# Kernel tuning notes

Measured on AMD Instinct MI355X. Metric: run time of the kernel, lower is better.

The kernel has to match this reference:

```python
import jax, jax.numpy as jnp
import numpy as np
import math

DIM = 512
HEADS = 8          # dim // num_head_channels = 512 // 64
HEAD_CH = 64
GROUPS = 32        # guided-diffusion normalization() = GroupNorm(32, dim)
EPS = 1e-5
CROSS_DIM = 768


def setup_inputs() -> dict:
    key = jax.random.key(0)
    ks = jax.random.split(key, 8)
    B, C, Hs, Ws, L = 16, DIM, 32, 32, 77
    x = jax.random.normal(ks[0], (B, C, Hs, Ws), dtype=jnp.float32)
    c = jax.random.normal(ks[1], (B, CROSS_DIM, L), dtype=jnp.float32)
    # GroupNorm affine params
    gamma = jnp.ones((C,), jnp.float32)
    beta = jnp.zeros((C,), jnp.float32)
    # 1x1 conv weights stored as [out, in]
    w_qkv = jax.random.normal(ks[2], (3 * C, C), jnp.float32) / math.sqrt(C)
    b_qkv = jnp.zeros((3 * C,), jnp.float32)
    w_c = jax.random.normal(ks[3], (2 * C, CROSS_DIM), jnp.float32) / math.sqrt(CROSS_DIM)
    b_c = jnp.zeros((2 * C,), jnp.float32)
    # NOTE: original proj_out is zero-initialized (zero_module); we use small
    # random weights so the reference exercises non-trivial math end-to-end.
    w_p = jax.random.normal(ks[4], (C, C), jnp.float32) / math.sqrt(C)
    b_p = jnp.zeros((C,), jnp.float32)
    return {"x": x, "c": c, "gamma": gamma, "beta": beta,
            "w_qkv": w_qkv, "b_qkv": b_qkv, "w_c": w_c, "b_c": b_c,
            "w_p": w_p, "b_p": b_p}


def reference(x, c, gamma, beta, w_qkv, b_qkv, w_c, b_c, w_p, b_p):
    B, C, Hs, Ws = x.shape
    T = Hs * Ws
    xf = x.reshape(B, C, T)

    # GroupNorm(32) over (channels_per_group, spatial)
    xg = xf.reshape(B, GROUPS, C // GROUPS, T)
    mean = xg.mean(axis=(2, 3), keepdims=True)
    var = xg.var(axis=(2, 3), keepdims=True)
    xn = ((xg - mean) * jax.lax.rsqrt(var + EPS)).reshape(B, C, T)
    xn = xn * gamma[None, :, None] + beta[None, :, None]

    # qkv 1x1 conv: [B, 3C, T]
    qkv = jnp.einsum('oc,bct->bot', w_qkv, xn) + b_qkv[None, :, None]
    q, k, v = jnp.split(qkv, 3, axis=1)
    q = q.reshape(B, HEADS, HEAD_CH, T)
    k = k.reshape(B, HEADS, HEAD_CH, T)
    v = v.reshape(B, HEADS, HEAD_CH, T)

    # cross-attn cond kv: [B, 2C, L] -> concat on sequence axis
    ckv = jnp.einsum('oc,bcl->bol', w_c, c) + b_c[None, :, None]
    kc, vc = jnp.split(ckv, 2, axis=1)
    L = c.shape[-1]
    k = jnp.concatenate([k, kc.reshape(B, HEADS, HEAD_CH, L)], axis=-1)
    v = jnp.concatenate([v, vc.reshape(B, HEADS, HEAD_CH, L)], axis=-1)

    scale = 1.0 / math.sqrt(HEAD_CH)
    # scores [B, H, T, T+L]; scale applied inside softmax as in FusedSoftmaxMaybeApex
    logits = jnp.einsum('bhct,bhcs->bhts', q, k) * scale
    w = jax.nn.softmax(logits, axis=-1)
    a = jnp.einsum('bhts,bhcs->bhct', w, v).reshape(B, C, T)

    h = jnp.einsum('oc,bct->bot', w_p, a) + b_p[None, :, None]
    return (xf + h).reshape(B, C, Hs, Ws)
```

## Files before the change

kernel.cpp:

```cpp
#include <hip/hip_runtime.h>

#define B_   16
#define C_   512
#define T_   1024
#define H_   8
#define D_   64
#define G_   32
#define L_   77
#define S_   1101
#define SPAD 1152
#define NPAD 51
#define CD_  768
#define BT_  (B_*T_)
#define BL_  (B_*L_)
#define KROW 72
#define QSC  0.18033688011112042f

typedef __bf16 bf16x8 __attribute__((ext_vector_type(8)));
typedef float  f32x4  __attribute__((ext_vector_type(4)));

static __device__ __forceinline__ unsigned short f2bf(float f) {
    unsigned int u = __float_as_uint(f);
    u = (u + 0x7fffu + ((u >> 16) & 1u)) >> 16;
    return (unsigned short)u;
}

static __device__ __forceinline__ void gload_lds16(const unsigned short* g,
                                                   unsigned short* l) {
    __builtin_amdgcn_global_load_lds(
        (const __attribute__((address_space(1))) unsigned int*)g,
        (__attribute__((address_space(3))) unsigned int*)l, 16, 0, 0);
}

__global__ __launch_bounds__(256) void prep_k(const float* __restrict__ x,
                                              float* __restrict__ stats,
                                              const float* __restrict__ w_qkv,
                                              const float* __restrict__ w_p,
                                              const float* __restrict__ w_c,
                                              unsigned short* __restrict__ wqkv_pk,
                                              unsigned short* __restrict__ wp_pk,
                                              unsigned short* __restrict__ wc_pk) {
    const int tid = threadIdx.x;
    if (blockIdx.x < 512) {
        const int bg = blockIdx.x;
        const float* p = x + (size_t)bg * 16384;
        float s = 0.f, s2 = 0.f;
        for (int i = tid; i < 16384; i += 256) {
            float v = p[i];
            s += v; s2 += v * v;
        }
        __shared__ float rs[256], rs2[256];
        rs[tid] = s; rs2[tid] = s2;
        __syncthreads();
        for (int off = 128; off > 0; off >>= 1) {
            if (tid < off) { rs[tid] += rs[tid + off]; rs2[tid] += rs2[tid + off]; }
            __syncthreads();
        }
        if (tid == 0) {
            float mean = rs[0] * (1.0f / 16384.0f);
            float var  = rs2[0] * (1.0f / 16384.0f) - mean * mean;
            stats[2 * bg]     = mean;
            stats[2 * bg + 1] = rsqrtf(var + 1e-5f);
        }
        return;
    }
    const int cid = (blockIdx.x - 512) * 256 + tid;
    const float* src;
    unsigned short* dst;
    if (cid < 98304) {
        const int ml = cid & 127, k8 = (cid >> 7) & 7, kt = (cid >> 10) & 7, mt = cid >> 13;
        src = w_qkv + (size_t)(mt * 128 + ml) * 512 + kt * 64 + k8 * 8;
        dst = wqkv_pk + (size_t)cid * 8;
    } else if (cid < 131072) {
        const int c2 = cid - 98304;
        const int ml = c2 & 127, k8 = (c2 >> 7) & 7, kt = (c2 >> 10) & 7, mt = c2 >> 13;
        src = w_p + (size_t)(mt * 128 + ml) * 512 + kt * 64 + k8 * 8;
        dst = wp_pk + (size_t)c2 * 8;
    } else {
        const int c3 = cid - 131072;
        const int ml = c3 & 127, k8 = (c3 >> 7) & 7;
        const int ktmt = c3 >> 10;
        const int kt = ktmt % 12, mt = ktmt / 12;
        src = w_c + (size_t)(mt * 128 + ml) * 768 + kt * 64 + k8 * 8;
        dst = wc_pk + (size_t)c3 * 8;
    }
    const float4 v0 = *(const float4*)src, v1 = *(const float4*)(src + 4);
    unsigned short tmp[8];
    tmp[0] = f2bf(v0.x); tmp[1] = f2bf(v0.y); tmp[2] = f2bf(v0.z); tmp[3] = f2bf(v0.w);
    tmp[4] = f2bf(v1.x); tmp[5] = f2bf(v1.y); tmp[6] = f2bf(v1.z); tmp[7] = f2bf(v1.w);
    *(uint4*)dst = *(uint4*)tmp;
}

__global__ __launch_bounds__(256) void gn_apply_t(const float* __restrict__ x,
                                                  const float* __restrict__ stats,
                                                  const float* __restrict__ gamma,
                                                  const float* __restrict__ beta,
                                                  unsigned short* __restrict__ xnT) {
    const int t0 = blockIdx.x * 64, kt = blockIdx.y, b = blockIdx.z;
    const int c0 = kt * 64;
    const int tid = threadIdx.x;
    __shared__ float st[64][66];
#pragma unroll
    for (int it = 0; it < 4; it++) {
        const int fid = it * 256 + tid;
        const int ci = fid >> 4, t4 = (fid & 15) * 4;
        const int c = c0 + ci;
        const float4 xv = *(const float4*)&x[((size_t)(b * C_ + c) << 10) + t0 + t4];
        const int bg = b * G_ + (c >> 4);
        const float mean = stats[2 * bg], istd = stats[2 * bg + 1];
        const float gs = gamma[c] * istd, gb = beta[c] - mean * gs;
        st[t4 + 0][ci] = xv.x * gs + gb;
        st[t4 + 1][ci] = xv.y * gs + gb;
        st[t4 + 2][ci] = xv.z * gs + gb;
        st[t4 + 3][ci] = xv.w * gs + gb;
    }
    __syncthreads();
#pragma unroll
    for (int it = 0; it < 2; it++) {
        const int cid = it * 256 + tid;
        const int k8 = cid >> 6, tl = cid & 63;
        const int n = (b << 10) + t0 + tl;
        const int nt = n >> 7, nm = n & 127;
        unsigned short tmp[8];
        const float* src = &st[tl][k8 * 8];
#pragma unroll
        for (int q = 0; q < 8; q++) tmp[q] = f2bf(src[q]);
        *(uint4*)&xnT[(((size_t)nt * 8 + kt) * 8 + k8) * 1024 + (size_t)nm * 8] = *(uint4*)tmp;
    }
}

__global__ __launch_bounds__(256) void pack_c_k(const float* __restrict__ c,
                                                unsigned short* __restrict__ cpk) {
    const int kt = blockIdx.x, b = blockIdx.y;
#pragma unroll
    for (int it = 0; it < 4; it++) {
        const int idx = it * 256 + threadIdx.x;
        const int k8 = idx >> 7, l = idx & 127;
        unsigned short tmp[8];
        const float* src = c + ((size_t)b * CD_ + kt * 64 + k8 * 8) * L_ + l;
#pragma unroll
        for (int q = 0; q < 8; q++)
            tmp[q] = (l < L_) ? f2bf(src[(size_t)q * L_]) : (unsigned short)0;
        *(uint4*)&cpk[(size_t)b * 98304 + ((size_t)(kt * 8 + k8)) * 1024 + (size_t)l * 8] =
            *(uint4*)tmp;
    }
}

template<int MODE, int KT>
__global__ __launch_bounds__(256) void mgemm_k(const unsigned short* __restrict__ Apk,
                                               const unsigned short* __restrict__ Bpk,
                                               const float* __restrict__ bias,
                                               const float* __restrict__ resid,
                                               unsigned short* __restrict__ qb,
                                               unsigned short* __restrict__ kb,
                                               unsigned short* __restrict__ vb,
                                               float* __restrict__ outp) {
    __shared__ unsigned short lds[16896];
    const int tid = threadIdx.x, wave = tid >> 6, lane = tid & 63;
    const int quad = lane >> 4, l16 = lane & 15;
    const int nt = blockIdx.x, mt = blockIdx.y;
    const int mw = (wave & 1) * 64, nw = (wave >> 1) * 64;

    f32x4 acc[4][4];
#pragma unroll
    for (int i = 0; i < 4; i++)
#pragma unroll
        for (int j = 0; j < 4; j++) acc[i][j] = (f32x4){0.f, 0.f, 0.f, 0.f};

    const unsigned short* Ab = Apk + (size_t)mt * KT * 8192;
    const unsigned short* Bb = Bpk + ((MODE == 2) ? (size_t)blockIdx.z * KT * 8192 : 0)
                                   + (size_t)nt * KT * 8192;

    for (int kt = 0; kt < KT; kt++) {
        const unsigned short* as = Ab + kt * 8192 + wave * 2048 + lane * 8;
        const unsigned short* bs = Bb + kt * 8192 + wave * 2048 + lane * 8;
        unsigned short* la = lds + wave * 2048;
        unsigned short* lb = lds + 8192 + wave * 2048;
#pragma unroll
        for (int j = 0; j < 4; j++) {
            gload_lds16(as + j * 512, la + j * 512);
            gload_lds16(bs + j * 512, lb + j * 512);
        }
        __syncthreads();
#pragma unroll
        for (int kh = 0; kh < 2; kh++) {
            const int k8 = kh * 4 + quad;
            bf16x8 af[4], bfr[4];
#pragma unroll
            for (int i = 0; i < 4; i++) {
                af[i]  = *(const bf16x8*)&lds[(size_t)(k8 * 128 + mw + i * 16 + l16) * 8];
                bfr[i] = *(const bf16x8*)&lds[8192 + (size_t)(k8 * 128 + nw + i * 16 + l16) * 8];
            }
#pragma unroll
            for (int mi = 0; mi < 4; mi++)
#pragma unroll
                for (int ni = 0; ni < 4; ni++)
                    acc[mi][ni] = __builtin_amdgcn_mfma_f32_16x16x32_bf16(
                        af[mi], bfr[ni], acc[mi][ni], 0, 0, 0);
        }
        __syncthreads();
    }

    const int gm0 = mt * 128 + mw;
    const int gn0 = nt * 128 + nw;

    if (MODE == 0) {
        const int region = gm0 >> 9;
        const int o0 = gm0 & 511;
        const int h = o0 >> 6;
        const int b = gn0 >> 10, t0 = gn0 & 1023;
        const int bh = b * 8 + h;
        unsigned short* wlds = lds + wave * 4224;
        if (region < 2) {
            const float sc = (region == 0) ? QSC : 1.0f;
#pragma unroll
            for (int mi = 0; mi < 4; mi++)
#pragma unroll
                for (int ni = 0; ni < 4; ni++)
#pragma unroll
                    for (int r = 0; r < 4; r++) {
                        const float v = (acc[mi][ni][r] + bias[gm0 + mi * 16 + quad * 4 + r]) * sc;
                        wlds[(ni * 16 + l16) * 66 + mi * 16 + quad * 4 + r] = f2bf(v);
                    }
            __syncthreads();
            unsigned short* dst = (region == 0)
                ? qb + ((size_t)bh * 1024 + t0) * 64
                : kb + ((size_t)bh * SPAD + t0) * 64;
            const int ch8 = lane & 7, tb = lane >> 3;
#pragma unroll
            for (int it = 0; it < 8; it++) {
                const int tl = it * 8 + tb;
                *(uint4*)&dst[(size_t)tl * 64 + ch8 * 8] = *(const uint4*)&wlds[tl * 66 + ch8 * 8];
            }
        } else {
#pragma unroll
            for (int mi = 0; mi < 4; mi++)
#pragma unroll
                for (int ni = 0; ni < 4; ni++)
#pragma unroll
                    for (int r = 0; r < 4; r++) {
                        const float v = acc[mi][ni][r] + bias[gm0 + mi * 16 + quad * 4 + r];
                        wlds[(mi * 16 + quad * 4 + r) * 66 + ni * 16 + l16] = f2bf(v);
                    }
            __syncthreads();
            const int s8 = lane & 7, cb = lane >> 3;
#pragma unroll
            for (int it = 0; it < 8; it++) {
                const int ch = it * 8 + cb;
                *(uint4*)&vb[((size_t)bh * 64 + ch) * SPAD + t0 + s8 * 8] =
                    *(const uint4*)&wlds[ch * 66 + s8 * 8];
            }
        }
    } else if (MODE == 1) {
        const int b = gn0 >> 10, t0 = gn0 & 1023;
#pragma unroll
        for (int mi = 0; mi < 4; mi++) {
#pragma unroll
            for (int r = 0; r < 4; r++) {
                const int m = gm0 + mi * 16 + quad * 4 + r;
                const float bv = bias[m];
                const size_t rowb = ((size_t)(b * C_ + m) << 10) + t0;
#pragma unroll
                for (int ni = 0; ni < 4; ni++) {
                    const size_t a = rowb + ni * 16 + l16;
                    outp[a] = acc[mi][ni][r] + bv + resid[a];
                }
            }
        }
    } else {
        const int region = gm0 >> 9;
        const int o0 = gm0 & 511;
        const int h = o0 >> 6;
        const int b = blockIdx.z;
        const int bh = b * 8 + h;
        unsigned short* wlds = lds + wave * 4224;
        if (region == 0) {
#pragma unroll
            for (int mi = 0; mi < 4; mi++)
#pragma unroll
                for (int ni = 0; ni < 4; ni++) {
                    const bool valid = (gn0 + ni * 16 + l16) < L_;
#pragma unroll
                    for (int r = 0; r < 4; r++) {
                        const float v = valid ? acc[mi][ni][r] + bias[gm0 + mi * 16 + quad * 4 + r] : 0.f;
                        wlds[(ni * 16 + l16) * 66 + mi * 16 + quad * 4 + r] = f2bf(v);
                    }
                }
            __syncthreads();
            unsigned short* dst = kb + ((size_t)bh * SPAD + 1024 + gn0) * 64;
            const int ch8 = lane & 7, tb = lane >> 3;
#pragma unroll
            for (int it = 0; it < 8; it++) {
                const int tl = it * 8 + tb;
                *(uint4*)&dst[(size_t)tl * 64 + ch8 * 8] = *(const uint4*)&wlds[tl * 66 + ch8 * 8];
            }
        } else {
#pragma unroll
            for (int mi = 0; mi < 4; mi++)
#pragma unroll
                for (int ni = 0; ni < 4; ni++) {
                    const bool valid = (gn0 + ni * 16 + l16) < L_;
#pragma unroll
                    for (int r = 0; r < 4; r++) {
                        const float v = valid ? acc[mi][ni][r] + bias[gm0 + mi * 16 + quad * 4 + r] : 0.f;
                        wlds[(mi * 16 + quad * 4 + r) * 66 + ni * 16 + l16] = f2bf(v);
                    }
                }
            __syncthreads();
            const int s8 = lane & 7, cb = lane >> 3;
#pragma unroll
            for (int it = 0; it < 8; it++) {
                const int ch = it * 8 + cb;
                *(uint4*)&vb[((size_t)bh * 64 + ch) * SPAD + 1024 + gn0 + s8 * 8] =
                    *(const uint4*)&wlds[ch * 66 + s8 * 8];
            }
        }
    }
}

__global__ __launch_bounds__(256) void flash_k(const unsigned short* __restrict__ qb,
                                               const unsigned short* __restrict__ kb,
                                               const unsigned short* __restrict__ vb,
                                               unsigned short* __restrict__ aT) {
    __shared__ __align__(16) unsigned short qs[64 * KROW];
    __shared__ __align__(16) unsigned short ks[64 * KROW];
    __shared__ __align__(16) unsigned short vs[64 * KROW];

    const int tid  = threadIdx.x;
    const int wave = tid >> 6, lane = tid & 63;
    const int quad = lane >> 4, l16 = lane & 15;
    const int bh  = blockIdx.x;
    const int b = bh >> 3, h = bh & 7;
    const int qt0 = blockIdx.y * 64;

    {
        const int row = tid >> 2, col = (tid & 3) * 16;
        const unsigned short* src = qb + ((size_t)bh * 1024 + qt0) * 64;
        *(uint4*)&qs[row * KROW + col]     = *(const uint4*)&src[row * 64 + col];
        *(uint4*)&qs[row * KROW + col + 8] = *(const uint4*)&src[row * 64 + col + 8];
    }
    const int qrow = wave * 16 + l16;
    const bf16x8 aq0 = *(const bf16x8*)&qs[qrow * KROW + quad * 8];
    const bf16x8 aq1 = *(const bf16x8*)&qs[qrow * KROW + 32 + quad * 8];

    unsigned short* ps = qs + wave * 16 * KROW;

    float rsum[4] = {0.f, 0.f, 0.f, 0.f};
    f32x4 o_acc[4];
#pragma unroll
    for (int nb = 0; nb < 4; nb++) o_acc[nb] = (f32x4){0.f, 0.f, 0.f, 0.f};

    for (int s0 = 0; s0 < SPAD; s0 += 64) {
        __syncthreads();
        {
            const int row = tid >> 2, col = (tid & 3) * 16;
            const unsigned short* ksrc = kb + ((size_t)bh * SPAD + s0 + row) * 64;
            *(uint4*)&ks[row * KROW + col]     = *(const uint4*)&ksrc[col];
            *(uint4*)&ks[row * KROW + col + 8] = *(const uint4*)&ksrc[col + 8];
            const unsigned short* vsrc = vb + ((size_t)bh * 64 + row) * SPAD + s0;
            *(uint4*)&vs[row * KROW + col]     = *(const uint4*)&vsrc[col];
            *(uint4*)&vs[row * KROW + col + 8] = *(const uint4*)&vsrc[col + 8];
        }
        __syncthreads();

        f32x4 sacc[4];
#pragma unroll
        for (int cb = 0; cb < 4; cb++) {
            const bf16x8 bk0 = *(const bf16x8*)&ks[(cb * 16 + l16) * KROW + quad * 8];
            const bf16x8 bk1 = *(const bf16x8*)&ks[(cb * 16 + l16) * KROW + 32 + quad * 8];
            f32x4 z = (f32x4){0.f, 0.f, 0.f, 0.f};
            z = __builtin_amdgcn_mfma_f32_16x16x32_bf16(aq0, bk0, z, 0, 0, 0);
            z = __builtin_amdgcn_mfma_f32_16x16x32_bf16(aq1, bk1, z, 0, 0, 0);
            sacc[cb] = z;
        }

#pragma unroll
        for (int cb = 0; cb < 4; cb++) {
#pragma unroll
            for (int r = 0; r < 4; r++) {
                const float e = __builtin_exp2f(sacc[cb][r]);
                rsum[r] += e;
                ps[(quad * 4 + r) * 64 + ((cb * 16 + l16 + 16 * quad) & 63)] = f2bf(e);
            }
        }
        asm volatile("s_waitcnt lgkmcnt(0)" ::: "memory");

        const int pc0 = (quad * 8 + 16 * (l16 >> 2)) & 63;
        const int pc1 = (32 + quad * 8 + 16 * (l16 >> 2)) & 63;
        const bf16x8 ap0 = *(const bf16x8*)&ps[l16 * 64 + pc0];
        const bf16x8 ap1 = *(const bf16x8*)&ps[l16 * 64 + pc1];
#pragma unroll
        for (int nb = 0; nb < 4; nb++) {
            const bf16x8 bv0 = *(const bf16x8*)&vs[(nb * 16 + l16) * KROW + quad * 8];
            const bf16x8 bv1 = *(const bf16x8*)&vs[(nb * 16 + l16) * KROW + 32 + quad * 8];
            o_acc[nb] = __builtin_amdgcn_mfma_f32_16x16x32_bf16(ap0, bv0, o_acc[nb], 0, 0, 0);
            o_acc[nb] = __builtin_amdgcn_mfma_f32_16x16x32_bf16(ap1, bv1, o_acc[nb], 0, 0, 0);
        }
    }

    float linv[4];
#pragma unroll
    for (int r = 0; r < 4; r++) {
        float s = rsum[r];
#pragma unroll
        for (int off = 1; off < 16; off <<= 1) s += __shfl_xor(s, off);
        linv[r] = 1.0f / (s - (float)NPAD);
    }

#pragma unroll
    for (int nb = 0; nb < 4; nb++) {
#pragma unroll
        for (int r = 0; r < 4; r++)
            ps[(quad * 4 + r) * 64 + ((nb * 16 + l16 + 16 * quad) & 63)] =
                f2bf(o_acc[nb][r] * linv[r]);
    }
    asm volatile("s_waitcnt lgkmcnt(0)" ::: "memory");
    const int k8 = lane >> 3;
#pragma unroll
    for (int it = 0; it < 2; it++) {
        const int tl = (lane & 7) + it * 8;
        const int pc = (k8 * 8 + 16 * (tl >> 2)) & 63;
        const int n = (b << 10) + qt0 + wave * 16 + tl;
        const int ntb = n >> 7, nm = n & 127;
        *(uint4*)&aT[(((size_t)ntb * 8 + h) * 8 + k8) * 1024 + (size_t)nm * 8] =
            *(const uint4*)&ps[tl * 64 + pc];
    }
}

extern "C" void kernel_launch(void* const* d_in, const int* in_sizes, int n_in,
                              void* d_out, int out_size, void* d_ws, size_t ws_size,
                              hipStream_t stream) {
    const float* x     = (const float*)d_in[0];
    const float* cin   = (const float*)d_in[1];
    const float* gamma = (const float*)d_in[2];
    const float* beta  = (const float*)d_in[3];
    const float* w_qkv = (const float*)d_in[4];
    const float* b_qkv = (const float*)d_in[5];
    const float* w_c   = (const float*)d_in[6];
    const float* b_c   = (const float*)d_in[7];
    const float* w_p   = (const float*)d_in[8];
    const float* b_p   = (const float*)d_in[9];
    float* out = (float*)d_out;

    float* ws    = (float*)d_ws;
    float* stats = ws;
    unsigned short* xnT     = (unsigned short*)(ws + 1024);
    unsigned short* wqkv_pk = xnT + 8388608;
    unsigned short* wp_pk   = wqkv_pk + 786432;
    unsigned short* wc_pk   = wp_pk + 262144;
    unsigned short* cpk     = wc_pk + 786432;
    unsigned short* qb      = cpk + 1572864;
    unsigned short* kb      = qb + 8388608;
    unsigned short* vb      = kb + 9437184;
    unsigned short* aT      = vb + 9437184;

    prep_k<<<dim3(512 + 896), 256, 0, stream>>>(x, stats, w_qkv, w_p, w_c,
                                                wqkv_pk, wp_pk, wc_pk);
    gn_apply_t<<<dim3(16, 8, 16), 256, 0, stream>>>(x, stats, gamma, beta, xnT);
    pack_c_k<<<dim3(12, 16), 256, 0, stream>>>(cin, cpk);
    mgemm_k<0, 8><<<dim3(128, 12), 256, 0, stream>>>(wqkv_pk, xnT, b_qkv, nullptr,
                                                     qb, kb, vb, nullptr);
    mgemm_k<2, 12><<<dim3(1, 8, 16), 256, 0, stream>>>(wc_pk, cpk, b_c, nullptr,
                                                       nullptr, kb, vb, nullptr);
    flash_k<<<dim3(128, 16), 256, 0, stream>>>(qb, kb, vb, aT);
    mgemm_k<1, 8><<<dim3(128, 4), 256, 0, stream>>>(wp_pk, aT, b_p, x,
                                                    nullptr, nullptr, nullptr, out);
}
```

Measured before the change: 324.8 us.

## Store Q/K/V in MFMA-packed tiles and stream K/V via direct LDS loads

```diff
diff --git a/kernel.cpp b/kernel.cpp
--- a/kernel.cpp
+++ b/kernel.cpp
@@ -12,8 +12,7 @@
 #define NPAD 51
 #define CD_  768
 #define BT_  (B_*T_)
-#define BL_  (B_*L_)
-#define KROW 72
+#define SROW 72
 #define QSC  0.18033688011112042f
 
 typedef __bf16 bf16x8 __attribute__((ext_vector_type(8)));
@@ -23,6 +22,12 @@
     unsigned int u = __float_as_uint(f);
     u = (u + 0x7fffu + ((u >> 16) & 1u)) >> 16;
     return (unsigned short)u;
+}
+
+static __device__ __forceinline__ unsigned int pk_bf16(float a, float b) {
+    unsigned int d;
+    asm("v_cvt_pk_bf16_f32 %0, %1, %2" : "=v"(d) : "v"(a), "v"(b));
+    return d;
 }
 
 static __device__ __forceinline__ void gload_lds16(const unsigned short* g,
@@ -37,9 +42,11 @@
                                               const float* __restrict__ w_qkv,
                                               const float* __restrict__ w_p,
                                               const float* __restrict__ w_c,
+                                              const float* __restrict__ cin,
                                               unsigned short* __restrict__ wqkv_pk,
                                               unsigned short* __restrict__ wp_pk,
-                                              unsigned short* __restrict__ wc_pk) {
+                                              unsigned short* __restrict__ wc_pk,
+                                              unsigned short* __restrict__ cpk) {
     const int tid = threadIdx.x;
     if (blockIdx.x < 512) {
         const int bg = blockIdx.x;
@@ -64,31 +71,48 @@
         }
         return;
     }
-    const int cid = (blockIdx.x - 512) * 256 + tid;
-    const float* src;
-    unsigned short* dst;
-    if (cid < 98304) {
-        const int ml = cid & 127, k8 = (cid >> 7) & 7, kt = (cid >> 10) & 7, mt = cid >> 13;
-        src = w_qkv + (size_t)(mt * 128 + ml) * 512 + kt * 64 + k8 * 8;
-        dst = wqkv_pk + (size_t)cid * 8;
-    } else if (cid < 131072) {
-        const int c2 = cid - 98304;
-        const int ml = c2 & 127, k8 = (c2 >> 7) & 7, kt = (c2 >> 10) & 7, mt = c2 >> 13;
-        src = w_p + (size_t)(mt * 128 + ml) * 512 + kt * 64 + k8 * 8;
-        dst = wp_pk + (size_t)c2 * 8;
-    } else {
-        const int c3 = cid - 131072;
-        const int ml = c3 & 127, k8 = (c3 >> 7) & 7;
-        const int ktmt = c3 >> 10;
-        const int kt = ktmt % 12, mt = ktmt / 12;
-        src = w_c + (size_t)(mt * 128 + ml) * 768 + kt * 64 + k8 * 8;
-        dst = wc_pk + (size_t)c3 * 8;
-    }
-    const float4 v0 = *(const float4*)src, v1 = *(const float4*)(src + 4);
-    unsigned short tmp[8];
-    tmp[0] = f2bf(v0.x); tmp[1] = f2bf(v0.y); tmp[2] = f2bf(v0.z); tmp[3] = f2bf(v0.w);
-    tmp[4] = f2bf(v1.x); tmp[5] = f2bf(v1.y); tmp[6] = f2bf(v1.z); tmp[7] = f2bf(v1.w);
-    *(uint4*)dst = *(uint4*)tmp;
+    if (blockIdx.x < 1408) {
+        const int cid = (blockIdx.x - 512) * 256 + tid;
+        const float* src;
+        unsigned short* dst;
+        if (cid < 98304) {
+            const int ml = cid & 127, k8 = (cid >> 7) & 7, kt = (cid >> 10) & 7, mt = cid >> 13;
+            src = w_qkv + (size_t)(mt * 128 + ml) * 512 + kt * 64 + k8 * 8;
+            dst = wqkv_pk + (size_t)cid * 8;
+        } else if (cid < 131072) {
+            const int c2 = cid - 98304;
+            const int ml = c2 & 127, k8 = (c2 >> 7) & 7, kt = (c2 >> 10) & 7, mt = c2 >> 13;
+            src = w_p + (size_t)(mt * 128 + ml) * 512 + kt * 64 + k8 * 8;
+            dst = wp_pk + (size_t)c2 * 8;
+        } else {
+            const int c3 = cid - 131072;
+            const int ml = c3 & 127, k8 = (c3 >> 7) & 7;
+            const int ktmt = c3 >> 10;
+            const int kt = ktmt % 12, mt = ktmt / 12;
+            src = w_c + (size_t)(mt * 128 + ml) * 768 + kt * 64 + k8 * 8;
+            dst = wc_pk + (size_t)c3 * 8;
+        }
+        const float4 v0 = *(const float4*)src, v1 = *(const float4*)(src + 4);
+        unsigned short tmp[8];
+        tmp[0] = f2bf(v0.x); tmp[1] = f2bf(v0.y); tmp[2] = f2bf(v0.z); tmp[3] = f2bf(v0.w);
+        tmp[4] = f2bf(v1.x); tmp[5] = f2bf(v1.y); tmp[6] = f2bf(v1.z); tmp[7] = f2bf(v1.w);
+        *(uint4*)dst = *(uint4*)tmp;
+        return;
+    }
+    const int idx2 = blockIdx.x - 1408;
+    const int kt = idx2 % 12, b = idx2 / 12;
+#pragma unroll
+    for (int it = 0; it < 4; it++) {
+        const int idx = it * 256 + tid;
+        const int k8 = idx >> 7, l = idx & 127;
+        unsigned short tmp[8];
+        const float* src = cin + ((size_t)b * CD_ + kt * 64 + k8 * 8) * L_ + l;
+#pragma unroll
+        for (int q = 0; q < 8; q++)
+            tmp[q] = (l < L_) ? f2bf(src[(size_t)q * L_]) : (unsigned short)0;
+        *(uint4*)&cpk[(size_t)b * 98304 + ((size_t)(kt * 8 + k8)) * 1024 + (size_t)l * 8] =
+            *(uint4*)tmp;
+    }
 }
 
 __global__ __launch_bounds__(256) void gn_apply_t(const float* __restrict__ x,
@@ -129,33 +153,16 @@
     }
 }
 
-__global__ __launch_bounds__(256) void pack_c_k(const float* __restrict__ c,
-                                                unsigned short* __restrict__ cpk) {
-    const int kt = blockIdx.x, b = blockIdx.y;
-#pragma unroll
-    for (int it = 0; it < 4; it++) {
-        const int idx = it * 256 + threadIdx.x;
-        const int k8 = idx >> 7, l = idx & 127;
-        unsigned short tmp[8];
-        const float* src = c + ((size_t)b * CD_ + kt * 64 + k8 * 8) * L_ + l;
-#pragma unroll
-        for (int q = 0; q < 8; q++)
-            tmp[q] = (l < L_) ? f2bf(src[(size_t)q * L_]) : (unsigned short)0;
-        *(uint4*)&cpk[(size_t)b * 98304 + ((size_t)(kt * 8 + k8)) * 1024 + (size_t)l * 8] =
-            *(uint4*)tmp;
-    }
-}
-
 template<int MODE, int KT>
 __global__ __launch_bounds__(256) void mgemm_k(const unsigned short* __restrict__ Apk,
                                                const unsigned short* __restrict__ Bpk,
                                                const float* __restrict__ bias,
                                                const float* __restrict__ resid,
-                                               unsigned short* __restrict__ qb,
-                                               unsigned short* __restrict__ kb,
-                                               unsigned short* __restrict__ vb,
+                                               unsigned short* __restrict__ qpk,
+                                               unsigned short* __restrict__ kpk,
+                                               unsigned short* __restrict__ vpk,
                                                float* __restrict__ outp) {
-    __shared__ unsigned short lds[16896];
+    __shared__ unsigned short lds[18432];
     const int tid = threadIdx.x, wave = tid >> 6, lane = tid & 63;
     const int quad = lane >> 4, l16 = lane & 15;
     const int nt = blockIdx.x, mt = blockIdx.y;
@@ -204,54 +211,7 @@
     const int gm0 = mt * 128 + mw;
     const int gn0 = nt * 128 + nw;
 
-    if (MODE == 0) {
-        const int region = gm0 >> 9;
-        const int o0 = gm0 & 511;
-        const int h = o0 >> 6;
-        const int b = gn0 >> 10, t0 = gn0 & 1023;
-        const int bh = b * 8 + h;
-        unsigned short* wlds = lds + wave * 4224;
-        if (region < 2) {
-            const float sc = (region == 0) ? QSC : 1.0f;
-#pragma unroll
-            for (int mi = 0; mi < 4; mi++)
-#pragma unroll
-                for (int ni = 0; ni < 4; ni++)
-#pragma unroll
-                    for (int r = 0; r < 4; r++) {
-                        const float v = (acc[mi][ni][r] + bias[gm0 + mi * 16 + quad * 4 + r]) * sc;
-                        wlds[(ni * 16 + l16) * 66 + mi * 16 + quad * 4 + r] = f2bf(v);
-                    }
-            __syncthreads();
-            unsigned short* dst = (region == 0)
-                ? qb + ((size_t)bh * 1024 + t0) * 64
-                : kb + ((size_t)bh * SPAD + t0) * 64;
-            const int ch8 = lane & 7, tb = lane >> 3;
-#pragma unroll
-            for (int it = 0; it < 8; it++) {
-                const int tl = it * 8 + tb;
-                *(uint4*)&dst[(size_t)tl * 64 + ch8 * 8] = *(const uint4*)&wlds[tl * 66 + ch8 * 8];
-            }
-        } else {
-#pragma unroll
-            for (int mi = 0; mi < 4; mi++)
-#pragma unroll
-                for (int ni = 0; ni < 4; ni++)
-#pragma unroll
-                    for (int r = 0; r < 4; r++) {
-                        const float v = acc[mi][ni][r] + bias[gm0 + mi * 16 + quad * 4 + r];
-                        wlds[(mi * 16 + quad * 4 + r) * 66 + ni * 16 + l16] = f2bf(v);
-                    }
-            __syncthreads();
-            const int s8 = lane & 7, cb = lane >> 3;
-#pragma unroll
-            for (int it = 0; it < 8; it++) {
-                const int ch = it * 8 + cb;
-                *(uint4*)&vb[((size_t)bh * 64 + ch) * SPAD + t0 + s8 * 8] =
-                    *(const uint4*)&wlds[ch * 66 + s8 * 8];
-            }
-        }
-    } else if (MODE == 1) {
+    if (MODE == 1) {
         const int b = gn0 >> 10, t0 = gn0 & 1023;
 #pragma unroll
         for (int mi = 0; mi < 4; mi++) {
@@ -267,64 +227,91 @@
                 }
             }
         }
+        return;
+    }
+
+    const int region = gm0 >> 9;
+    const int h = (gm0 & 511) >> 6;
+    const int b = (MODE == 2) ? blockIdx.z : (gn0 >> 10);
+    const int bh = b * 8 + h;
+    const bool vregion = (MODE == 0) ? (region == 2) : (region == 1);
+
+    if (!vregion) {
+        const float sc = (MODE == 0 && region == 0) ? QSC : 1.0f;
+        unsigned short* base;
+        int trow0;
+        size_t tilestride;
+        if (MODE == 0) {
+            base = (region == 0) ? qpk + (size_t)bh * 16 * 4096
+                                 : kpk + (size_t)bh * 18 * 4096;
+            trow0 = gn0 & 1023;
+        } else {
+            base = kpk + (size_t)(bh * 18 + 16 + (gn0 >> 6)) * 4096;
+            trow0 = -1;
+        }
+        (void)tilestride;
+#pragma unroll
+        for (int mi = 0; mi < 4; mi++) {
+            const int k8 = mi * 2 + (quad >> 1);
+            const int sub = (quad & 1) * 4;
+#pragma unroll
+            for (int ni = 0; ni < 4; ni++) {
+                float vv[4];
+                bool valid = true;
+                if (MODE == 2) valid = (gn0 + ni * 16 + l16) < L_;
+#pragma unroll
+                for (int r = 0; r < 4; r++)
+                    vv[r] = valid ? (acc[mi][ni][r] + bias[gm0 + mi * 16 + quad * 4 + r]) * sc
+                                  : 0.f;
+                uint2 d;
+                d.x = pk_bf16(vv[0], vv[1]);
+                d.y = pk_bf16(vv[2], vv[3]);
+                unsigned short* dst;
+                if (MODE == 0) {
+                    const int t = trow0 + ni * 16 + l16;
+                    dst = base + (size_t)(t >> 6) * 4096 + ((size_t)k8 * 64 + (t & 63)) * 8 + sub;
+                } else {
+                    const int row = ni * 16 + l16;
+                    dst = base + ((size_t)k8 * 64 + row) * 8 + sub;
+                }
+                *(uint2*)dst = d;
+            }
+        }
     } else {
-        const int region = gm0 >> 9;
-        const int o0 = gm0 & 511;
-        const int h = o0 >> 6;
-        const int b = blockIdx.z;
-        const int bh = b * 8 + h;
-        unsigned short* wlds = lds + wave * 4224;
-        if (region == 0) {
-#pragma unroll
-            for (int mi = 0; mi < 4; mi++)
-#pragma unroll
-                for (int ni = 0; ni < 4; ni++) {
-                    const bool valid = (gn0 + ni * 16 + l16) < L_;
-#pragma unroll
-                    for (int r = 0; r < 4; r++) {
-                        const float v = valid ? acc[mi][ni][r] + bias[gm0 + mi * 16 + quad * 4 + r] : 0.f;
-                        wlds[(ni * 16 + l16) * 66 + mi * 16 + quad * 4 + r] = f2bf(v);
-                    }
+        unsigned short* wlds = lds + wave * 4608;
+#pragma unroll
+        for (int mi = 0; mi < 4; mi++)
+#pragma unroll
+            for (int ni = 0; ni < 4; ni++) {
+                bool valid = true;
+                if (MODE == 2) valid = (gn0 + ni * 16 + l16) < L_;
+#pragma unroll
+                for (int r = 0; r < 4; r++) {
+                    const float v = valid ? acc[mi][ni][r] + bias[gm0 + mi * 16 + quad * 4 + r]
+                                          : 0.f;
+                    wlds[(mi * 16 + quad * 4 + r) * SROW + ni * 16 + l16] = f2bf(v);
                 }
-            __syncthreads();
-            unsigned short* dst = kb + ((size_t)bh * SPAD + 1024 + gn0) * 64;
-            const int ch8 = lane & 7, tb = lane >> 3;
-#pragma unroll
-            for (int it = 0; it < 8; it++) {
-                const int tl = it * 8 + tb;
-                *(uint4*)&dst[(size_t)tl * 64 + ch8 * 8] = *(const uint4*)&wlds[tl * 66 + ch8 * 8];
             }
-        } else {
-#pragma unroll
-            for (int mi = 0; mi < 4; mi++)
-#pragma unroll
-                for (int ni = 0; ni < 4; ni++) {
-                    const bool valid = (gn0 + ni * 16 + l16) < L_;
-#pragma unroll
-                    for (int r = 0; r < 4; r++) {
-                        const float v = valid ? acc[mi][ni][r] + bias[gm0 + mi * 16 + quad * 4 + r] : 0.f;
-                        wlds[(mi * 16 + quad * 4 + r) * 66 + ni * 16 + l16] = f2bf(v);
-                    }
-                }
-            __syncthreads();
-            const int s8 = lane & 7, cb = lane >> 3;
-#pragma unroll
-            for (int it = 0; it < 8; it++) {
-                const int ch = it * 8 + cb;
-                *(uint4*)&vb[((size_t)bh * 64 + ch) * SPAD + 1024 + gn0 + s8 * 8] =
-                    *(const uint4*)&wlds[ch * 66 + s8 * 8];
-            }
-        }
-    }
-}
-
-__global__ __launch_bounds__(256) void flash_k(const unsigned short* __restrict__ qb,
-                                               const unsigned short* __restrict__ kb,
-                                               const unsigned short* __restrict__ vb,
+        __syncthreads();
+        const int stile = (MODE == 0) ? ((gn0 & 1023) >> 6) : (16 + (gn0 >> 6));
+        unsigned short* dst = vpk + (size_t)(bh * 18 + stile) * 4096;
+        const int sk8 = lane & 7, cb = lane >> 3;
+#pragma unroll
+        for (int it = 0; it < 8; it++) {
+            const int ch = it * 8 + cb;
+            *(uint4*)&dst[((size_t)sk8 * 64 + ch) * 8] =
+                *(const uint4*)&wlds[ch * SROW + sk8 * 8];
+        }
+    }
+}
+
+__global__ __launch_bounds__(256) void flash_k(const unsigned short* __restrict__ qpk,
+                                               const unsigned short* __restrict__ kpk,
+                                               const unsigned short* __restrict__ vpk,
                                                unsigned short* __restrict__ aT) {
-    __shared__ __align__(16) unsigned short qs[64 * KROW];
-    __shared__ __align__(16) unsigned short ks[64 * KROW];
-    __shared__ __align__(16) unsigned short vs[64 * KROW];
+    __shared__ __align__(16) unsigned short ks[4096];
+    __shared__ __align__(16) unsigned short vs[4096];
+    __shared__ __align__(16) unsigned short psA[4 * 16 * SROW];
 
     const int tid  = threadIdx.x;
     const int wave = tid >> 6, lane = tid & 63;
@@ -333,97 +320,88 @@
     const int b = bh >> 3, h = bh & 7;
     const int qt0 = blockIdx.y * 64;
 
-    {
-        const int row = tid >> 2, col = (tid & 3) * 16;
-        const unsigned short* src = qb + ((size_t)bh * 1024 + qt0) * 64;
-        *(uint4*)&qs[row * KROW + col]     = *(const uint4*)&src[row * 64 + col];
-        *(uint4*)&qs[row * KROW + col + 8] = *(const uint4*)&src[row * 64 + col + 8];
-    }
+    const unsigned short* qtb = qpk + ((size_t)bh * 16 + blockIdx.y) * 4096;
     const int qrow = wave * 16 + l16;
-    const bf16x8 aq0 = *(const bf16x8*)&qs[qrow * KROW + quad * 8];
-    const bf16x8 aq1 = *(const bf16x8*)&qs[qrow * KROW + 32 + quad * 8];
-
-    unsigned short* ps = qs + wave * 16 * KROW;
-
-    float rsum[4] = {0.f, 0.f, 0.f, 0.f};
+    const bf16x8 bq0 = *(const bf16x8*)&qtb[((size_t)quad * 64 + qrow) * 8];
+    const bf16x8 bq1 = *(const bf16x8*)&qtb[((size_t)(quad + 4) * 64 + qrow) * 8];
+
+    unsigned short* ps = psA + wave * 16 * SROW;
+
+    float rsum = 0.f;
     f32x4 o_acc[4];
 #pragma unroll
     for (int nb = 0; nb < 4; nb++) o_acc[nb] = (f32x4){0.f, 0.f, 0.f, 0.f};
 
-    for (int s0 = 0; s0 < SPAD; s0 += 64) {
-        __syncthreads();
-        {
-            const int row = tid >> 2, col = (tid & 3) * 16;
-            const unsigned short* ksrc = kb + ((size_t)bh * SPAD + s0 + row) * 64;
-            *(uint4*)&ks[row * KROW + col]     = *(const uint4*)&ksrc[col];
-            *(uint4*)&ks[row * KROW + col + 8] = *(const uint4*)&ksrc[col + 8];
-            const unsigned short* vsrc = vb + ((size_t)bh * 64 + row) * SPAD + s0;
-            *(uint4*)&vs[row * KROW + col]     = *(const uint4*)&vsrc[col];
-            *(uint4*)&vs[row * KROW + col + 8] = *(const uint4*)&vsrc[col + 8];
-        }
+    for (int stile = 0; stile < 18; stile++) {
+        const unsigned short* kt = kpk + ((size_t)bh * 18 + stile) * 4096 + wave * 1024 + lane * 8;
+        const unsigned short* vt = vpk + ((size_t)bh * 18 + stile) * 4096 + wave * 1024 + lane * 8;
+        unsigned short* lk = ks + wave * 1024;
+        unsigned short* lv = vs + wave * 1024;
+        gload_lds16(kt, lk);       gload_lds16(kt + 512, lk + 512);
+        gload_lds16(vt, lv);       gload_lds16(vt + 512, lv + 512);
         __syncthreads();
 
         f32x4 sacc[4];
 #pragma unroll
-        for (int cb = 0; cb < 4; cb++) {
-            const bf16x8 bk0 = *(const bf16x8*)&ks[(cb * 16 + l16) * KROW + quad * 8];
-            const bf16x8 bk1 = *(const bf16x8*)&ks[(cb * 16 + l16) * KROW + 32 + quad * 8];
+        for (int sb = 0; sb < 4; sb++) {
+            const bf16x8 ak0 = *(const bf16x8*)&ks[((size_t)quad * 64 + sb * 16 + l16) * 8];
+            const bf16x8 ak1 = *(const bf16x8*)&ks[((size_t)(quad + 4) * 64 + sb * 16 + l16) * 8];
             f32x4 z = (f32x4){0.f, 0.f, 0.f, 0.f};
-            z = __builtin_amdgcn_mfma_f32_16x16x32_bf16(aq0, bk0, z, 0, 0, 0);
-            z = __builtin_amdgcn_mfma_f32_16x16x32_bf16(aq1, bk1, z, 0, 0, 0);
-            sacc[cb] = z;
-        }
-
-#pragma unroll
-        for (int cb = 0; cb < 4; cb++) {
-#pragma unroll
-            for (int r = 0; r < 4; r++) {
-                const float e = __builtin_exp2f(sacc[cb][r]);
-                rsum[r] += e;
-                ps[(quad * 4 + r) * 64 + ((cb * 16 + l16 + 16 * quad) & 63)] = f2bf(e);
-            }
+            z = __builtin_amdgcn_mfma_f32_16x16x32_bf16(ak0, bq0, z, 0, 0, 0);
+            z = __builtin_amdgcn_mfma_f32_16x16x32_bf16(ak1, bq1, z, 0, 0, 0);
+            sacc[sb] = z;
+        }
+
+#pragma unroll
+        for (int sb = 0; sb < 4; sb++) {
+            const float e0 = __builtin_exp2f(sacc[sb][0]);
+            const float e1 = __builtin_exp2f(sacc[sb][1]);
+            const float e2 = __builtin_exp2f(sacc[sb][2]);
+            const float e3 = __builtin_exp2f(sacc[sb][3]);
+            rsum += (e0 + e1) + (e2 + e3);
+            uint2 d;
+            d.x = pk_bf16(e0, e1);
+            d.y = pk_bf16(e2, e3);
+            *(uint2*)&ps[l16 * SROW + sb * 16 + quad * 4] = d;
         }
         asm volatile("s_waitcnt lgkmcnt(0)" ::: "memory");
 
-        const int pc0 = (quad * 8 + 16 * (l16 >> 2)) & 63;
-        const int pc1 = (32 + quad * 8 + 16 * (l16 >> 2)) & 63;
-        const bf16x8 ap0 = *(const bf16x8*)&ps[l16 * 64 + pc0];
-        const bf16x8 ap1 = *(const bf16x8*)&ps[l16 * 64 + pc1];
+        const bf16x8 ap0 = *(const bf16x8*)&ps[l16 * SROW + quad * 8];
+        const bf16x8 ap1 = *(const bf16x8*)&ps[l16 * SROW + 32 + quad * 8];
 #pragma unroll
         for (int nb = 0; nb < 4; nb++) {
-            const bf16x8 bv0 = *(const bf16x8*)&vs[(nb * 16 + l16) * KROW + quad * 8];
-            const bf16x8 bv1 = *(const bf16x8*)&vs[(nb * 16 + l16) * KROW + 32 + quad * 8];
+            const bf16x8 bv0 = *(const bf16x8*)&vs[((size_t)quad * 64 + nb * 16 + l16) * 8];
+            const bf16x8 bv1 = *(const bf16x8*)&vs[((size_t)(quad + 4) * 64 + nb * 16 + l16) * 8];
             o_acc[nb] = __builtin_amdgcn_mfma_f32_16x16x32_bf16(ap0, bv0, o_acc[nb], 0, 0, 0);
             o_acc[nb] = __builtin_amdgcn_mfma_f32_16x16x32_bf16(ap1, bv1, o_acc[nb], 0, 0, 0);
         }
-    }
-
+        __syncthreads();
+    }
+
+    float lsum = rsum;
+    lsum += __shfl_xor(lsum, 16);
+    lsum += __shfl_xor(lsum, 32);
     float linv[4];
 #pragma unroll
     for (int r = 0; r < 4; r++) {
-        float s = rsum[r];
-#pragma unroll
-        for (int off = 1; off < 16; off <<= 1) s += __shfl_xor(s, off);
-        linv[r] = 1.0f / (s - (float)NPAD);
-    }
-
-#pragma unroll
-    for (int nb = 0; nb < 4; nb++) {
+        const float lr = __shfl(lsum, quad * 4 + r);
+        linv[r] = 1.0f / (lr - (float)NPAD);
+    }
+
+#pragma unroll
+    for (int nb = 0; nb < 4; nb++)
 #pragma unroll
         for (int r = 0; r < 4; r++)
-            ps[(quad * 4 + r) * 64 + ((nb * 16 + l16 + 16 * quad) & 63)] =
-                f2bf(o_acc[nb][r] * linv[r]);
-    }
+            ps[(quad * 4 + r) * SROW + nb * 16 + l16] = f2bf(o_acc[nb][r] * linv[r]);
     asm volatile("s_waitcnt lgkmcnt(0)" ::: "memory");
     const int k8 = lane >> 3;
 #pragma unroll
     for (int it = 0; it < 2; it++) {
         const int tl = (lane & 7) + it * 8;
-        const int pc = (k8 * 8 + 16 * (tl >> 2)) & 63;
         const int n = (b << 10) + qt0 + wave * 16 + tl;
         const int ntb = n >> 7, nm = n & 127;
         *(uint4*)&aT[(((size_t)ntb * 8 + h) * 8 + k8) * 1024 + (size_t)nm * 8] =
-            *(const uint4*)&ps[tl * 64 + pc];
+            *(const uint4*)&ps[tl * SROW + k8 * 8];
     }
 }
 
@@ -449,20 +427,19 @@
     unsigned short* wp_pk   = wqkv_pk + 786432;
     unsigned short* wc_pk   = wp_pk + 262144;
     unsigned short* cpk     = wc_pk + 786432;
-    unsigned short* qb      = cpk + 1572864;
-    unsigned short* kb      = qb + 8388608;
-    unsigned short* vb      = kb + 9437184;
-    unsigned short* aT      = vb + 9437184;
-
-    prep_k<<<dim3(512 + 896), 256, 0, stream>>>(x, stats, w_qkv, w_p, w_c,
-                                                wqkv_pk, wp_pk, wc_pk);
+    unsigned short* qpk     = cpk + 1572864;
+    unsigned short* kpk     = qpk + 8388608;
+    unsigned short* vpk     = kpk + 9437184;
+    unsigned short* aT      = vpk + 9437184;
+
+    prep_k<<<dim3(1600), 256, 0, stream>>>(x, stats, w_qkv, w_p, w_c, cin,
+                                           wqkv_pk, wp_pk, wc_pk, cpk);
     gn_apply_t<<<dim3(16, 8, 16), 256, 0, stream>>>(x, stats, gamma, beta, xnT);
-    pack_c_k<<<dim3(12, 16), 256, 0, stream>>>(cin, cpk);
     mgemm_k<0, 8><<<dim3(128, 12), 256, 0, stream>>>(wqkv_pk, xnT, b_qkv, nullptr,
-                                                     qb, kb, vb, nullptr);
+                                                     qpk, kpk, vpk, nullptr);
     mgemm_k<2, 12><<<dim3(1, 8, 16), 256, 0, stream>>>(wc_pk, cpk, b_c, nullptr,
-                                                       nullptr, kb, vb, nullptr);
-    flash_k<<<dim3(128, 16), 256, 0, stream>>>(qb, kb, vb, aT);
+                                                       nullptr, kpk, vpk, nullptr);
+    flash_k<<<dim3(128, 16), 256, 0, stream>>>(qpk, kpk, vpk, aT);
     mgemm_k<1, 8><<<dim3(128, 4), 256, 0, stream>>>(wp_pk, aT, b_p, x,
                                                     nullptr, nullptr, nullptr, out);
 }
```

Result: faster. 282.6 us (-13.0%).
